# Kernel optimization log

Measured on AMD Instinct MI355X. Metric: run time of the kernel, lower is better.

Reference implementation:

```python
import jax, jax.numpy as jnp
import numpy as np

EPS = 1e-5

def conv2d(x, w, b):
    # x: [B,C,H,W], w: [O,I,kh,kw], VALID padding, stride 1
    y = jax.lax.conv_general_dilated(x, w, (1, 1), 'VALID',
                                     dimension_numbers=('NCHW', 'OIHW', 'NCHW'))
    return y + b[None, :, None, None]

def batchnorm(x, g, b):
    # training-mode BN: batch statistics over (N,H,W), biased variance (torch semantics)
    m = jnp.mean(x, axis=(0, 2, 3), keepdims=True)
    v = jnp.mean((x - m) ** 2, axis=(0, 2, 3), keepdims=True)
    return g[None, :, None, None] * (x - m) / jnp.sqrt(v + EPS) + b[None, :, None, None]

def maxpool2(x):
    return jax.lax.reduce_window(x, -jnp.inf, jax.lax.max,
                                 (1, 1, 2, 2), (1, 1, 2, 2), 'VALID')

def self_attention(x, qw, qb, kw, kb, vw, vb, gamma):
    # x: [B,C,H,W]; qw/kw: [C//8, C]; vw: [C, C] (1x1 convs)
    B, C, H, W = x.shape
    xf = x.reshape(B, C, H * W)                               # [B,C,N]
    q = jnp.einsum('oc,bcn->bon', qw, xf) + qb[None, :, None]  # [B,C//8,N]
    k = jnp.einsum('oc,bcn->bon', kw, xf) + kb[None, :, None]
    v = jnp.einsum('oc,bcn->bon', vw, xf) + vb[None, :, None]  # [B,C,N]
    energy = jnp.einsum('bcn,bcm->bnm', q, k)                  # [B,N,N] (query n, key m)
    attn = jax.nn.softmax(energy, axis=-1)
    out = jnp.einsum('bcm,bnm->bcn', v, attn)                  # [B,C,N]
    return gamma * out.reshape(B, C, H, W) + x

def setup_inputs() -> dict:
    key = jax.random.key(0)
    ks = jax.random.split(key, 20)
    s = 0.05
    d = {}
    d['x'] = jax.random.normal(ks[0], (1, 3, 256, 256), jnp.float32)
    d['conv1_w'] = jax.random.normal(ks[1], (32, 3, 3, 3), jnp.float32) * s
    d['conv1_b'] = jnp.zeros((32,), jnp.float32)
    d['bn1_g'] = jnp.ones((32,), jnp.float32)
    d['bn1_b'] = jnp.zeros((32,), jnp.float32)
    d['a1_qw'] = jax.random.normal(ks[2], (4, 32), jnp.float32) * s
    d['a1_qb'] = jnp.zeros((4,), jnp.float32)
    d['a1_kw'] = jax.random.normal(ks[3], (4, 32), jnp.float32) * s
    d['a1_kb'] = jnp.zeros((4,), jnp.float32)
    d['a1_vw'] = jax.random.normal(ks[4], (32, 32), jnp.float32) * s
    d['a1_vb'] = jnp.zeros((32,), jnp.float32)
    d['a1_gamma'] = jnp.ones((1,), jnp.float32)
    d['conv2_w'] = jax.random.normal(ks[5], (64, 32, 3, 3), jnp.float32) * s
    d['conv2_b'] = jnp.zeros((64,), jnp.float32)
    d['bn2_g'] = jnp.ones((64,), jnp.float32)
    d['bn2_b'] = jnp.zeros((64,), jnp.float32)
    d['a2_qw'] = jax.random.normal(ks[6], (8, 64), jnp.float32) * s
    d['a2_qb'] = jnp.zeros((8,), jnp.float32)
    d['a2_kw'] = jax.random.normal(ks[7], (8, 64), jnp.float32) * s
    d['a2_kb'] = jnp.zeros((8,), jnp.float32)
    d['a2_vw'] = jax.random.normal(ks[8], (64, 64), jnp.float32) * s
    d['a2_vb'] = jnp.zeros((64,), jnp.float32)
    d['a2_gamma'] = jnp.ones((1,), jnp.float32)
    d['fc_w'] = jax.random.normal(ks[9], (50, 64 * 62 * 62), jnp.float32) * 0.002
    d['fc_b'] = jnp.zeros((50,), jnp.float32)
    return d

def reference(x, conv1_w, conv1_b, bn1_g, bn1_b,
              a1_qw, a1_qb, a1_kw, a1_kb, a1_vw, a1_vb, a1_gamma,
              conv2_w, conv2_b, bn2_g, bn2_b,
              a2_qw, a2_qb, a2_kw, a2_kb, a2_vw, a2_vb, a2_gamma,
              fc_w, fc_b):
    h = conv2d(x, conv1_w, conv1_b)                 # [B,32,254,254]
    h = jax.nn.relu(batchnorm(h, bn1_g, bn1_b))
    h = maxpool2(h)                                 # [B,32,127,127]
    h = self_attention(h, a1_qw, a1_qb, a1_kw, a1_kb, a1_vw, a1_vb, a1_gamma)
    h = conv2d(h, conv2_w, conv2_b)                 # [B,64,125,125]
    h = jax.nn.relu(batchnorm(h, bn2_g, bn2_b))
    h = maxpool2(h)                                 # [B,64,62,62]
    h = self_attention(h, a2_qw, a2_qb, a2_kw, a2_kb, a2_vw, a2_vb, a2_gamma)
    h = h.reshape(h.shape[0], -1)                   # [B, 64*62*62]
    return h @ fc_w.T + fc_b
```

## Files before the change

kernel.cpp:

```cpp
#include <hip/hip_runtime.h>
#include <hip/hip_bf16.h>

typedef float f32x4 __attribute__((ext_vector_type(4)));
typedef short bf16x4 __attribute__((ext_vector_type(4)));
typedef unsigned short u16x4 __attribute__((ext_vector_type(4)));
typedef unsigned short u16x8 __attribute__((ext_vector_type(8)));

__device__ inline unsigned short f2bf(float x) {
    __hip_bfloat16 h = __float2bfloat16(x);
    return *reinterpret_cast<unsigned short*>(&h);
}

__device__ inline int cvt_pk_bf16(float a, float b) {
    int r;
    asm("v_cvt_pk_bf16_f32 %0, %1, %2" : "=v"(r) : "v"(a), "v"(b));
    return r;
}

template <int CIN, int ICB>
__launch_bounds__(256)
__global__ void conv3x3_rt_kernel(const float* __restrict__ src, int H, int W,
                                  const float* __restrict__ w,
                                  const float* __restrict__ b,
                                  float* __restrict__ dst, int OH, int OW,
                                  float* __restrict__ bn_accum) {
    __shared__ __align__(16) float xs[ICB][18][68];
    __shared__ __align__(16) float wsm[ICB][12];
    __shared__ float red[512];

    const int oc  = blockIdx.z;
    const int ox0 = blockIdx.x * 64;
    const int oy0 = blockIdx.y * 16;
    const int tid = threadIdx.x;
    const int ty  = tid >> 4;
    const int tx  = (tid & 15) << 2;

    float o0, o1, o2, o3;
    o0 = o1 = o2 = o3 = b[oc];

    const int scol   = tid & 63;
    const int sslot0 = tid >> 6;
    const bool colok = (ox0 + scol) < W;

    for (int icb = 0; icb < CIN; icb += ICB) {
        __syncthreads();
        {
            int s  = sslot0;
            int rr = sslot0;
            const float* gp = src + ((size_t)icb * H + oy0 + rr) * W + ox0 + scol;
            float* lp = &xs[0][0][0] + (size_t)s * 68 + scol;
            while (s < ICB * 18) {
                int y = oy0 + rr;
                *lp = (y < H && colok) ? *gp : 0.f;
                s += 4; rr += 4;
                gp += 4 * (size_t)W;
                lp += 4 * 68;
                if (rr >= 18) { rr -= 18; gp += ((size_t)H - 18) * W; }
            }
        }
        if (tid < ICB * 18) {
            int c = tid / 18, r = tid - c * 18;
            int y = oy0 + r;
            const float* gp = src + ((size_t)(icb + c) * H + y) * W + ox0 + 64;
            bool yok = (y < H);
            xs[c][r][64] = (yok && (ox0 + 64) < W) ? gp[0] : 0.f;
            xs[c][r][65] = (yok && (ox0 + 65) < W) ? gp[1] : 0.f;
        }
        if (tid < ICB * 9) {
            int c = tid / 9, j = tid - c * 9;
            wsm[c][j] = w[((size_t)oc * CIN + icb + c) * 9 + j];
        }
        __syncthreads();

        #pragma unroll
        for (int c = 0; c < ICB; ++c) {
            float wv[9];
            #pragma unroll
            for (int j = 0; j < 9; ++j) wv[j] = wsm[c][j];
            #pragma unroll
            for (int kh = 0; kh < 3; ++kh) {
                const float* xp = &xs[c][ty + kh][tx];
                f32x4 x03 = *(const f32x4*)xp;
                float x4 = xp[4], x5 = xp[5];
                const float w0 = wv[kh * 3], w1 = wv[kh * 3 + 1], w2 = wv[kh * 3 + 2];
                o0 = fmaf(x03[0], w0, o0); o0 = fmaf(x03[1], w1, o0); o0 = fmaf(x03[2], w2, o0);
                o1 = fmaf(x03[1], w0, o1); o1 = fmaf(x03[2], w1, o1); o1 = fmaf(x03[3], w2, o1);
                o2 = fmaf(x03[2], w0, o2); o2 = fmaf(x03[3], w1, o2); o2 = fmaf(x4,     w2, o2);
                o3 = fmaf(x03[3], w0, o3); o3 = fmaf(x4,     w1, o3); o3 = fmaf(x5,     w2, o3);
            }
        }
    }

    const int oy = oy0 + ty;
    const int ox = ox0 + tx;
    float s1 = 0.f, s2 = 0.f;
    if (oy < OH) {
        float* dp = dst + ((size_t)oc * OH + oy) * OW + ox;
        if (ox + 0 < OW) { dp[0] = o0; s1 += o0; s2 = fmaf(o0, o0, s2); }
        if (ox + 1 < OW) { dp[1] = o1; s1 += o1; s2 = fmaf(o1, o1, s2); }
        if (ox + 2 < OW) { dp[2] = o2; s1 += o2; s2 = fmaf(o2, o2, s2); }
        if (ox + 3 < OW) { dp[3] = o3; s1 += o3; s2 = fmaf(o3, o3, s2); }
    }
    red[tid]       = s1;
    red[256 + tid] = s2;
    __syncthreads();
    for (int off2 = 128; off2 > 0; off2 >>= 1) {
        if (tid < off2) {
            red[tid]       += red[tid + off2];
            red[256 + tid] += red[256 + tid + off2];
        }
        __syncthreads();
    }
    if (tid == 0) {
        atomicAdd(&bn_accum[oc * 2],     red[0]);
        atomicAdd(&bn_accum[oc * 2 + 1], red[256]);
    }
}

__global__ void bn_final_kernel(const float* __restrict__ sums, int C, int spatial,
                                const float* __restrict__ g, const float* __restrict__ bb,
                                float* __restrict__ inv_shift) {
    int c = threadIdx.x;
    if (c >= C) return;
    float m   = sums[c * 2] / (float)spatial;
    float var = sums[c * 2 + 1] / (float)spatial - m * m;
    float inv = g[c] * rsqrtf(var + 1e-5f);
    inv_shift[c * 2]     = inv;
    inv_shift[c * 2 + 1] = bb[c] - m * inv;
}

__global__ void bn_pool_kernel(const float* __restrict__ src,
                               const float* __restrict__ inv_shift,
                               int H, int W, int OH, int OW, int C,
                               float* __restrict__ dst) {
    int i = blockIdx.x * blockDim.x + threadIdx.x;
    if (i >= C * OH * OW) return;
    int ox = i % OW;
    int oy = (i / OW) % OH;
    int c  = i / (OW * OH);
    float inv = inv_shift[c * 2], sh = inv_shift[c * 2 + 1];
    const float* p = src + ((size_t)c * H + 2 * oy) * W + 2 * ox;
    float a = fmaxf(fmaf(p[0],     inv, sh), 0.f);
    float b = fmaxf(fmaf(p[1],     inv, sh), 0.f);
    float d = fmaxf(fmaf(p[W],     inv, sh), 0.f);
    float e = fmaxf(fmaf(p[W + 1], inv, sh), 0.f);
    dst[i] = fmaxf(fmaxf(a, b), fmaxf(d, e));
}

__global__ void qkv_proj_kernel(const float* __restrict__ xf, int N, int NP, int C, int Cqk,
                                const float* __restrict__ qw, const float* __restrict__ qb,
                                const float* __restrict__ kw, const float* __restrict__ kb,
                                const float* __restrict__ vw, const float* __restrict__ vb,
                                unsigned short* __restrict__ qo,
                                unsigned short* __restrict__ ko,
                                unsigned short* __restrict__ vo) {
    constexpr int OCG = 8;
    __shared__ float wl[OCG * 64 + OCG];
    const int g0 = blockIdx.y * OCG;
    const int tid = threadIdx.x;
    for (int i = tid; i < OCG * C; i += blockDim.x) {
        int o = i / C, cc = i % C;
        int oc = g0 + o;
        const float* wsrc = (oc < Cqk) ? (qw + oc * C)
                          : (oc < 2 * Cqk) ? (kw + (oc - Cqk) * C)
                          : (vw + (oc - 2 * Cqk) * C);
        wl[o * C + cc] = wsrc[cc];
    }
    if (tid < OCG) {
        int oc = g0 + tid;
        wl[OCG * C + tid] = (oc < Cqk) ? qb[oc]
                          : (oc < 2 * Cqk) ? kb[oc - Cqk]
                          : vb[oc - 2 * Cqk];
    }
    __syncthreads();
    int n = blockIdx.x * blockDim.x + tid;
    if (n >= N) return;
    float acc[OCG];
    #pragma unroll
    for (int o = 0; o < OCG; ++o) acc[o] = wl[OCG * C + o];
    for (int c = 0; c < C; ++c) {
        float xv = xf[(size_t)c * N + n];
        #pragma unroll
        for (int o = 0; o < OCG; ++o) acc[o] = fmaf(xv, wl[o * C + c], acc[o]);
    }
    const float LOG2E = 1.44269504f;
    if (g0 < 2 * Cqk) {
        if (Cqk == 4) {
            u16x4 qs, ks;
            #pragma unroll
            for (int j = 0; j < 4; ++j) {
                qs[j] = f2bf(acc[j] * LOG2E);
                ks[j] = f2bf(acc[4 + j]);
            }
            *(u16x4*)&qo[(size_t)n * 4] = qs;
            *(u16x4*)&ko[(size_t)n * 4] = ks;
        } else {
            unsigned short* dst = (g0 == 0) ? qo : ko;
            float sc = (g0 == 0) ? LOG2E : 1.f;
            u16x4 a, bb2;
            #pragma unroll
            for (int j = 0; j < 4; ++j) {
                a[j]   = f2bf(acc[j] * sc);
                bb2[j] = f2bf(acc[4 + j] * sc);
            }
            *(u16x4*)&dst[(size_t)n * 8]     = a;
            *(u16x4*)&dst[(size_t)n * 8 + 4] = bb2;
        }
    } else {
        #pragma unroll
        for (int o = 0; o < OCG; ++o)
            vo[(size_t)(g0 + o - 2 * Cqk) * NP + n] = f2bf(acc[o]);
    }
}

template <int CQK, int CV>
__launch_bounds__(256)
__global__ void flash_mfma_kernel(const unsigned short* __restrict__ qbf,
                                  const unsigned short* __restrict__ kbf,
                                  const unsigned short* __restrict__ v,
                                  int N, int NP, int chunk,
                                  float* __restrict__ l_part,
                                  float* __restrict__ acc_part) {
    constexpr int VS = 72;
    __shared__ unsigned short vsm[2][CV * VS];
    const int tid  = threadIdx.x;
    const int wave = tid >> 6;
    const int lane = tid & 63;
    const int lq   = lane & 15;
    const int g    = lane >> 4;
    const int s    = blockIdx.y;
    const int m0   = s * chunk;
    const int m1   = min(N, m0 + chunk);
    const int qb   = blockIdx.x * 64 + wave * 16;
    const int n    = qb + lq;

    bf16x4 qf = (bf16x4){0, 0, 0, 0};
    if (g * 4 < CQK)
        qf = *(const bf16x4*)&qbf[(size_t)n * CQK + 4 * g];

    const int vch = tid >> 3;
    const int vkk = (tid & 7) * 8;

    f32x4 acc[CV / 16];
    #pragma unroll
    for (int f = 0; f < CV / 16; ++f) acc[f] = (f32x4){0.f, 0.f, 0.f, 0.f};
    float lsum = 0.f;

    const int nch = (m1 - m0 + 63) >> 6;

    u16x8 vreg[CV / 32];
    #pragma unroll
    for (int vv = 0; vv < CV / 32; ++vv)
        vreg[vv] = *(const u16x8*)&v[(size_t)(vch + 32 * vv) * NP + m0 + vkk];
    #pragma unroll
    for (int vv = 0; vv < CV / 32; ++vv)
        *(u16x8*)&vsm[0][(vch + 32 * vv) * VS + vkk] = vreg[vv];
    __syncthreads();

    for (int t = 0; t < nch; ++t) {
        const int mt  = m0 + t * 64;
        const int cur = t & 1;
        const int mtn = (t + 1 < nch) ? mt + 64 : mt;
        #pragma unroll
        for (int vv = 0; vv < CV / 32; ++vv)
            vreg[vv] = *(const u16x8*)&v[(size_t)(vch + 32 * vv) * NP + mtn + vkk];

        bf16x4 kf[4];
        #pragma unroll
        for (int tt = 0; tt < 4; ++tt) {
            kf[tt] = (bf16x4){0, 0, 0, 0};
            if (g * 4 < CQK)
                kf[tt] = *(const bf16x4*)&kbf[(size_t)(mt + 16 * tt + lq) * CQK + 4 * g];
        }
        f32x4 e[4];
        #pragma unroll
        for (int tt = 0; tt < 4; ++tt)
            e[tt] = __builtin_amdgcn_mfma_f32_16x16x16bf16_1k(
                kf[tt], qf, (f32x4){0.f, 0.f, 0.f, 0.f}, 0, 0, 0);

        bf16x4 pf[4];
        const bool tail = (mt + 64 > m1);
        if (!tail) {
            #pragma unroll
            for (int tt = 0; tt < 4; ++tt) {
                float p0 = exp2f(e[tt][0]), p1 = exp2f(e[tt][1]);
                float p2 = exp2f(e[tt][2]), p3 = exp2f(e[tt][3]);
                lsum += (p0 + p1) + (p2 + p3);
                int2 pi;
                pi.x = cvt_pk_bf16(p0, p1);
                pi.y = cvt_pk_bf16(p2, p3);
                pf[tt] = __builtin_bit_cast(bf16x4, pi);
            }
        } else {
            #pragma unroll
            for (int tt = 0; tt < 4; ++tt) {
                int key = mt + 16 * tt + 4 * g;
                float p0 = (key + 0 < m1) ? exp2f(e[tt][0]) : 0.f;
                float p1 = (key + 1 < m1) ? exp2f(e[tt][1]) : 0.f;
                float p2 = (key + 2 < m1) ? exp2f(e[tt][2]) : 0.f;
                float p3 = (key + 3 < m1) ? exp2f(e[tt][3]) : 0.f;
                lsum += (p0 + p1) + (p2 + p3);
                int2 pi;
                pi.x = cvt_pk_bf16(p0, p1);
                pi.y = cvt_pk_bf16(p2, p3);
                pf[tt] = __builtin_bit_cast(bf16x4, pi);
            }
        }

        #pragma unroll
        for (int tt = 0; tt < 4; ++tt) {
            #pragma unroll
            for (int f = 0; f < CV / 16; ++f) {
                bf16x4 vf = *(const bf16x4*)&vsm[cur][(f * 16 + lq) * VS + 16 * tt + 4 * g];
                acc[f] = __builtin_amdgcn_mfma_f32_16x16x16bf16_1k(pf[tt], vf, acc[f], 0, 0, 0);
            }
        }

        #pragma unroll
        for (int vv = 0; vv < CV / 32; ++vv)
            *(u16x8*)&vsm[cur ^ 1][(vch + 32 * vv) * VS + vkk] = vreg[vv];
        __syncthreads();
    }

    lsum += __shfl_xor(lsum, 16, 64);
    lsum += __shfl_xor(lsum, 32, 64);
    if (g == 0 && n < N) l_part[(size_t)s * N + n] = lsum;

    #pragma unroll
    for (int f = 0; f < CV / 16; ++f) {
        #pragma unroll
        for (int r2 = 0; r2 < 4; ++r2) {
            int nq = qb + 4 * g + r2;
            if (nq < N)
                acc_part[((size_t)s * N + nq) * CV + f * 16 + lq] = acc[f][r2];
        }
    }
}

__global__ void combine_kernel(const float* __restrict__ acc_part,
                               const float* __restrict__ l_part,
                               int nsplit, int N, int CV,
                               const float* __restrict__ gamma,
                               const float* __restrict__ x_res,
                               float* __restrict__ out) {
    int n = blockIdx.x * blockDim.x + threadIdx.x;
    if (n >= N) return;
    int cv0 = blockIdx.y * 16;
    float l = 0.f;
    for (int s = 0; s < nsplit; ++s) l += l_part[(size_t)s * N + n];
    f32x4 a[4];
    #pragma unroll
    for (int t = 0; t < 4; ++t) a[t] = (f32x4){0.f, 0.f, 0.f, 0.f};
    for (int s = 0; s < nsplit; ++s) {
        const float* p = acc_part + ((size_t)s * N + n) * CV + cv0;
        #pragma unroll
        for (int t = 0; t < 4; ++t) a[t] += *(const f32x4*)(p + 4 * t);
    }
    float gs = gamma[0] / l;
    #pragma unroll
    for (int t = 0; t < 4; ++t)
        #pragma unroll
        for (int u = 0; u < 4; ++u) {
            int cv = cv0 + 4 * t + u;
            out[(size_t)cv * N + n] = fmaf(gs, a[t][u], x_res[(size_t)cv * N + n]);
        }
}

__global__ void fc_partial_kernel(const float* __restrict__ h, const float* __restrict__ w,
                                  int K, int nchunk, float* __restrict__ partial) {
    const int r = blockIdx.y, cb = blockIdx.x;
    const int chunk = K / nchunk;
    const int j0 = cb * chunk;
    const int j1 = (cb == nchunk - 1) ? K : j0 + chunk;
    const float* wr = w + (size_t)r * K;
    float s = 0.f;
    for (int j = j0 + (int)threadIdx.x * 4; j + 3 < j1; j += blockDim.x * 4) {
        float4 hv = *reinterpret_cast<const float4*>(h + j);
        float4 wv = *reinterpret_cast<const float4*>(wr + j);
        s += hv.x * wv.x + hv.y * wv.y + hv.z * wv.z + hv.w * wv.w;
    }
    __shared__ float red[256];
    red[threadIdx.x] = s;
    __syncthreads();
    for (int off = 128; off > 0; off >>= 1) {
        if ((int)threadIdx.x < off) red[threadIdx.x] += red[threadIdx.x + off];
        __syncthreads();
    }
    if (threadIdx.x == 0) partial[r * gridDim.x + cb] = red[0];
}

__global__ void fc_final_kernel(const float* __restrict__ partial,
                                const float* __restrict__ b, int nchunk,
                                float* __restrict__ out) {
    int r = threadIdx.x;
    if (r < 50) {
        float s = b[r];
        for (int i = 0; i < nchunk; ++i) s += partial[r * nchunk + i];
        out[r] = s;
    }
}

extern "C" void kernel_launch(void* const* d_in, const int* in_sizes, int n_in,
                              void* d_out, int out_size, void* d_ws, size_t ws_size,
                              hipStream_t stream) {
    const float* x    = (const float*)d_in[0];
    const float* c1w  = (const float*)d_in[1];
    const float* c1b  = (const float*)d_in[2];
    const float* bn1g = (const float*)d_in[3];
    const float* bn1b = (const float*)d_in[4];
    const float* a1qw = (const float*)d_in[5];
    const float* a1qb = (const float*)d_in[6];
    const float* a1kw = (const float*)d_in[7];
    const float* a1kb = (const float*)d_in[8];
    const float* a1vw = (const float*)d_in[9];
    const float* a1vb = (const float*)d_in[10];
    const float* a1g  = (const float*)d_in[11];
    const float* c2w  = (const float*)d_in[12];
    const float* c2b  = (const float*)d_in[13];
    const float* bn2g = (const float*)d_in[14];
    const float* bn2b = (const float*)d_in[15];
    const float* a2qw = (const float*)d_in[16];
    const float* a2qb = (const float*)d_in[17];
    const float* a2kw = (const float*)d_in[18];
    const float* a2kb = (const float*)d_in[19];
    const float* a2vw = (const float*)d_in[20];
    const float* a2vb = (const float*)d_in[21];
    const float* a2g  = (const float*)d_in[22];
    const float* fcw  = (const float*)d_in[23];
    const float* fcb  = (const float*)d_in[24];
    float* out = (float*)d_out;

    const int N1 = 127 * 127;
    const int N2 = 62 * 62;
    const int NP1 = (N1 + 63) & ~63;
    const int NP2 = (N2 + 63) & ~63;
    const int NS1 = 4, NS2 = 16;
    const int CH1 = ((N1 + NS1 - 1) / NS1 + 63) & ~63;
    const int CH2 = ((N2 + NS2 - 1) / NS2 + 63) & ~63;

    char* base = (char*)d_ws;
    size_t off = 0;
    auto alloc = [&](size_t bytes) {
        void* p = base + off;
        off += (bytes + 63) & ~(size_t)63;
        return p;
    };
    float* h1     = (float*)alloc(sizeof(float) * 32 * 254 * 254);
    float* bnSums = (float*)alloc(sizeof(float) * 256);
    float* bnA    = (float*)alloc(sizeof(float) * 64);
    float* p1     = (float*)alloc(sizeof(float) * 32 * N1);
    unsigned short* q1 = (unsigned short*)alloc(sizeof(short) * NP1 * 4);
    unsigned short* k1 = (unsigned short*)alloc(sizeof(short) * NP1 * 4);
    unsigned short* v1 = (unsigned short*)alloc(sizeof(short) * 32 * NP1);
    float* l1     = (float*)alloc(sizeof(float) * NS1 * N1);
    float* a1p    = (float*)alloc(sizeof(float) * (size_t)NS1 * N1 * 32);
    float* ao1    = (float*)alloc(sizeof(float) * 32 * N1);
    float* h2     = (float*)alloc(sizeof(float) * 64 * 125 * 125);
    float* bnB    = (float*)alloc(sizeof(float) * 128);
    float* p2     = (float*)alloc(sizeof(float) * 64 * N2);
    unsigned short* q2 = (unsigned short*)alloc(sizeof(short) * NP2 * 8);
    unsigned short* k2 = (unsigned short*)alloc(sizeof(short) * NP2 * 8);
    unsigned short* v2 = (unsigned short*)alloc(sizeof(short) * 64 * NP2);
    float* l2     = (float*)alloc(sizeof(float) * NS2 * N2);
    float* a2p    = (float*)alloc(sizeof(float) * (size_t)NS2 * N2 * 64);
    float* ao2    = (float*)alloc(sizeof(float) * 64 * N2);
    float* fcp    = (float*)alloc(sizeof(float) * 2048);

    hipMemsetAsync(bnSums, 0, 256 * sizeof(float), stream);
    hipMemsetAsync(q1, 0, (char*)l1 - (char*)q1, stream);
    hipMemsetAsync(q2, 0, (char*)l2 - (char*)q2, stream);

    conv3x3_rt_kernel<3, 3><<<dim3(4, 16, 32), 256, 0, stream>>>(
        x, 256, 256, c1w, c1b, h1, 254, 254, bnSums);
    bn_final_kernel<<<1, 32, 0, stream>>>(bnSums, 32, 254 * 254, bn1g, bn1b, bnA);
    bn_pool_kernel<<<(32 * N1 + 255) / 256, 256, 0, stream>>>(
        h1, bnA, 254, 254, 127, 127, 32, p1);

    qkv_proj_kernel<<<dim3((N1 + 255) / 256, 5), 256, 0, stream>>>(
        p1, N1, NP1, 32, 4, a1qw, a1qb, a1kw, a1kb, a1vw, a1vb, q1, k1, v1);
    flash_mfma_kernel<4, 32><<<dim3((N1 + 63) / 64, NS1), 256, 0, stream>>>(
        q1, k1, v1, N1, NP1, CH1, l1, a1p);
    combine_kernel<<<dim3((N1 + 255) / 256, 2), 256, 0, stream>>>(
        a1p, l1, NS1, N1, 32, a1g, p1, ao1);

    conv3x3_rt_kernel<32, 8><<<dim3(2, 8, 64), 256, 0, stream>>>(
        ao1, 127, 127, c2w, c2b, h2, 125, 125, bnSums + 64);
    bn_final_kernel<<<1, 64, 0, stream>>>(bnSums + 64, 64, 125 * 125, bn2g, bn2b, bnB);
    bn_pool_kernel<<<(64 * N2 + 255) / 256, 256, 0, stream>>>(
        h2, bnB, 125, 125, 62, 62, 64, p2);

    qkv_proj_kernel<<<dim3((N2 + 255) / 256, 10), 256, 0, stream>>>(
        p2, N2, NP2, 64, 8, a2qw, a2qb, a2kw, a2kb, a2vw, a2vb, q2, k2, v2);
    flash_mfma_kernel<8, 64><<<dim3((N2 + 63) / 64, NS2), 256, 0, stream>>>(
        q2, k2, v2, N2, NP2, CH2, l2, a2p);
    combine_kernel<<<dim3((N2 + 255) / 256, 4), 256, 0, stream>>>(
        a2p, l2, NS2, N2, 64, a2g, p2, ao2);

    fc_partial_kernel<<<dim3(32, 50), 256, 0, stream>>>(ao2, fcw, 64 * N2, 32, fcp);
    fc_final_kernel<<<1, 64, 0, stream>>>(fcp, fcb, 32, out);
}
```

Measured before the change: 301.8 us.

## Process two query tiles per wave in flash attention to reuse K/V fragments

Measured after the change: 304.6 us. No clear change (+0.9%).

```diff
diff --git a/kernel.cpp b/kernel.cpp
--- a/kernel.cpp
+++ b/kernel.cpp
@@ -231,20 +231,27 @@
     const int s    = blockIdx.y;
     const int m0   = s * chunk;
     const int m1   = min(N, m0 + chunk);
-    const int qb   = blockIdx.x * 64 + wave * 16;
-    const int n    = qb + lq;
-
-    bf16x4 qf = (bf16x4){0, 0, 0, 0};
-    if (g * 4 < CQK)
-        qf = *(const bf16x4*)&qbf[(size_t)n * CQK + 4 * g];
+    const int qb0  = blockIdx.x * 128 + wave * 16;
+    const int n0   = qb0 + lq;
+    const int n1   = n0 + 64;
+
+    bf16x4 qf0 = (bf16x4){0, 0, 0, 0};
+    bf16x4 qf1 = (bf16x4){0, 0, 0, 0};
+    if (g * 4 < CQK) {
+        qf0 = *(const bf16x4*)&qbf[(size_t)n0 * CQK + 4 * g];
+        qf1 = *(const bf16x4*)&qbf[(size_t)n1 * CQK + 4 * g];
+    }
 
     const int vch = tid >> 3;
     const int vkk = (tid & 7) * 8;
 
-    f32x4 acc[CV / 16];
-    #pragma unroll
-    for (int f = 0; f < CV / 16; ++f) acc[f] = (f32x4){0.f, 0.f, 0.f, 0.f};
-    float lsum = 0.f;
+    f32x4 acc0[CV / 16], acc1[CV / 16];
+    #pragma unroll
+    for (int f = 0; f < CV / 16; ++f) {
+        acc0[f] = (f32x4){0.f, 0.f, 0.f, 0.f};
+        acc1[f] = (f32x4){0.f, 0.f, 0.f, 0.f};
+    }
+    float ls0 = 0.f, ls1 = 0.f;
 
     const int nch = (m1 - m0 + 63) >> 6;
 
@@ -272,38 +279,49 @@
             if (g * 4 < CQK)
                 kf[tt] = *(const bf16x4*)&kbf[(size_t)(mt + 16 * tt + lq) * CQK + 4 * g];
         }
-        f32x4 e[4];
-        #pragma unroll
-        for (int tt = 0; tt < 4; ++tt)
-            e[tt] = __builtin_amdgcn_mfma_f32_16x16x16bf16_1k(
-                kf[tt], qf, (f32x4){0.f, 0.f, 0.f, 0.f}, 0, 0, 0);
-
-        bf16x4 pf[4];
+        f32x4 e0[4], e1[4];
+        #pragma unroll
+        for (int tt = 0; tt < 4; ++tt) {
+            e0[tt] = __builtin_amdgcn_mfma_f32_16x16x16bf16_1k(
+                kf[tt], qf0, (f32x4){0.f, 0.f, 0.f, 0.f}, 0, 0, 0);
+            e1[tt] = __builtin_amdgcn_mfma_f32_16x16x16bf16_1k(
+                kf[tt], qf1, (f32x4){0.f, 0.f, 0.f, 0.f}, 0, 0, 0);
+        }
+
+        bf16x4 pf0[4], pf1[4];
         const bool tail = (mt + 64 > m1);
         if (!tail) {
             #pragma unroll
             for (int tt = 0; tt < 4; ++tt) {
-                float p0 = exp2f(e[tt][0]), p1 = exp2f(e[tt][1]);
-                float p2 = exp2f(e[tt][2]), p3 = exp2f(e[tt][3]);
-                lsum += (p0 + p1) + (p2 + p3);
-                int2 pi;
-                pi.x = cvt_pk_bf16(p0, p1);
-                pi.y = cvt_pk_bf16(p2, p3);
-                pf[tt] = __builtin_bit_cast(bf16x4, pi);
+                float a0 = exp2f(e0[tt][0]), a1 = exp2f(e0[tt][1]);
+                float a2 = exp2f(e0[tt][2]), a3 = exp2f(e0[tt][3]);
+                ls0 += (a0 + a1) + (a2 + a3);
+                int2 pi0; pi0.x = cvt_pk_bf16(a0, a1); pi0.y = cvt_pk_bf16(a2, a3);
+                pf0[tt] = __builtin_bit_cast(bf16x4, pi0);
+                float b0 = exp2f(e1[tt][0]), b1 = exp2f(e1[tt][1]);
+                float b2 = exp2f(e1[tt][2]), b3 = exp2f(e1[tt][3]);
+                ls1 += (b0 + b1) + (b2 + b3);
+                int2 pi1; pi1.x = cvt_pk_bf16(b0, b1); pi1.y = cvt_pk_bf16(b2, b3);
+                pf1[tt] = __builtin_bit_cast(bf16x4, pi1);
             }
         } else {
             #pragma unroll
             for (int tt = 0; tt < 4; ++tt) {
                 int key = mt + 16 * tt + 4 * g;
-                float p0 = (key + 0 < m1) ? exp2f(e[tt][0]) : 0.f;
-                float p1 = (key + 1 < m1) ? exp2f(e[tt][1]) : 0.f;
-                float p2 = (key + 2 < m1) ? exp2f(e[tt][2]) : 0.f;
-                float p3 = (key + 3 < m1) ? exp2f(e[tt][3]) : 0.f;
-                lsum += (p0 + p1) + (p2 + p3);
-                int2 pi;
-                pi.x = cvt_pk_bf16(p0, p1);
-                pi.y = cvt_pk_bf16(p2, p3);
-                pf[tt] = __builtin_bit_cast(bf16x4, pi);
+                float a0 = (key + 0 < m1) ? exp2f(e0[tt][0]) : 0.f;
+                float a1 = (key + 1 < m1) ? exp2f(e0[tt][1]) : 0.f;
+                float a2 = (key + 2 < m1) ? exp2f(e0[tt][2]) : 0.f;
+                float a3 = (key + 3 < m1) ? exp2f(e0[tt][3]) : 0.f;
+                ls0 += (a0 + a1) + (a2 + a3);
+                int2 pi0; pi0.x = cvt_pk_bf16(a0, a1); pi0.y = cvt_pk_bf16(a2, a3);
+                pf0[tt] = __builtin_bit_cast(bf16x4, pi0);
+                float b0 = (key + 0 < m1) ? exp2f(e1[tt][0]) : 0.f;
+                float b1 = (key + 1 < m1) ? exp2f(e1[tt][1]) : 0.f;
+                float b2 = (key + 2 < m1) ? exp2f(e1[tt][2]) : 0.f;
+                float b3 = (key + 3 < m1) ? exp2f(e1[tt][3]) : 0.f;
+                ls1 += (b0 + b1) + (b2 + b3);
+                int2 pi1; pi1.x = cvt_pk_bf16(b0, b1); pi1.y = cvt_pk_bf16(b2, b3);
+                pf1[tt] = __builtin_bit_cast(bf16x4, pi1);
             }
         }
 
@@ -312,7 +330,8 @@
             #pragma unroll
             for (int f = 0; f < CV / 16; ++f) {
                 bf16x4 vf = *(const bf16x4*)&vsm[cur][(f * 16 + lq) * VS + 16 * tt + 4 * g];
-                acc[f] = __builtin_amdgcn_mfma_f32_16x16x16bf16_1k(pf[tt], vf, acc[f], 0, 0, 0);
+                acc0[f] = __builtin_amdgcn_mfma_f32_16x16x16bf16_1k(pf0[tt], vf, acc0[f], 0, 0, 0);
+                acc1[f] = __builtin_amdgcn_mfma_f32_16x16x16bf16_1k(pf1[tt], vf, acc1[f], 0, 0, 0);
             }
         }
 
@@ -322,17 +341,25 @@
         __syncthreads();
     }
 
-    lsum += __shfl_xor(lsum, 16, 64);
-    lsum += __shfl_xor(lsum, 32, 64);
-    if (g == 0 && n < N) l_part[(size_t)s * N + n] = lsum;
+    ls0 += __shfl_xor(ls0, 16, 64);
+    ls0 += __shfl_xor(ls0, 32, 64);
+    ls1 += __shfl_xor(ls1, 16, 64);
+    ls1 += __shfl_xor(ls1, 32, 64);
+    if (g == 0) {
+        if (n0 < N) l_part[(size_t)s * N + n0] = ls0;
+        if (n1 < N) l_part[(size_t)s * N + n1] = ls1;
+    }
 
     #pragma unroll
     for (int f = 0; f < CV / 16; ++f) {
         #pragma unroll
         for (int r2 = 0; r2 < 4; ++r2) {
-            int nq = qb + 4 * g + r2;
-            if (nq < N)
-                acc_part[((size_t)s * N + nq) * CV + f * 16 + lq] = acc[f][r2];
+            int nq0 = qb0 + 4 * g + r2;
+            int nq1 = nq0 + 64;
+            if (nq0 < N)
+                acc_part[((size_t)s * N + nq0) * CV + f * 16 + lq] = acc0[f][r2];
+            if (nq1 < N)
+                acc_part[((size_t)s * N + nq1) * CV + f * 16 + lq] = acc1[f][r2];
         }
     }
 }
@@ -432,9 +459,9 @@
 
     const int N1 = 127 * 127;
     const int N2 = 62 * 62;
-    const int NP1 = (N1 + 63) & ~63;
-    const int NP2 = (N2 + 63) & ~63;
-    const int NS1 = 4, NS2 = 16;
+    const int NP1 = 16256;
+    const int NP2 = 3968;
+    const int NS1 = 8, NS2 = 16;
     const int CH1 = ((N1 + NS1 - 1) / NS1 + 63) & ~63;
     const int CH2 = ((N2 + NS2 - 1) / NS2 + 63) & ~63;
 
@@ -478,7 +505,7 @@
 
     qkv_proj_kernel<<<dim3((N1 + 255) / 256, 5), 256, 0, stream>>>(
         p1, N1, NP1, 32, 4, a1qw, a1qb, a1kw, a1kb, a1vw, a1vb, q1, k1, v1);
-    flash_mfma_kernel<4, 32><<<dim3((N1 + 63) / 64, NS1), 256, 0, stream>>>(
+    flash_mfma_kernel<4, 32><<<dim3((N1 + 127) / 128, NS1), 256, 0, stream>>>(
         q1, k1, v1, N1, NP1, CH1, l1, a1p);
     combine_kernel<<<dim3((N1 + 255) / 256, 2), 256, 0, stream>>>(
         a1p, l1, NS1, N1, 32, a1g, p1, ao1);
@@ -491,7 +518,7 @@
 
     qkv_proj_kernel<<<dim3((N2 + 255) / 256, 10), 256, 0, stream>>>(
         p2, N2, NP2, 64, 8, a2qw, a2qb, a2kw, a2kb, a2vw, a2vb, q2, k2, v2);
-    flash_mfma_kernel<8, 64><<<dim3((N2 + 63) / 64, NS2), 256, 0, stream>>>(
+    flash_mfma_kernel<8, 64><<<dim3((N2 + 127) / 128, NS2), 256, 0, stream>>>(
         q2, k2, v2, N2, NP2, CH2, l2, a2p);
     combine_kernel<<<dim3((N2 + 255) / 256, 4), 256, 0, stream>>>(
         a2p, l2, NS2, N2, 64, a2g, p2, ao2);
```
